# Kernel tuning notes

Measured on AMD Instinct MI355X. Metric: run time of the kernel, lower is better.

## Reference

```python
import jax, jax.numpy as jnp
import numpy as np

B, S, D, H = 4, 1024, 1024, 16
HS = D // H  # head_size = 64


def setup_inputs() -> dict:
    key = jax.random.key(0)
    ks = jax.random.split(key, 6)
    scale = 1.0 / np.sqrt(D)
    data = jax.random.normal(ks[0], (B, S, D), dtype=jnp.float32)
    # Per-head projection weights, stacked: [H, D, HS] (no bias, per nn.Linear(bias=False))
    Wq = jax.random.normal(ks[1], (H, D, HS), dtype=jnp.float32) * scale
    Wk = jax.random.normal(ks[2], (H, D, HS), dtype=jnp.float32) * scale
    Wv = jax.random.normal(ks[3], (H, D, HS), dtype=jnp.float32) * scale
    # Output projection: [H*HS, D] plus bias [D]
    Wo = jax.random.normal(ks[4], (H * HS, D), dtype=jnp.float32) * scale
    bo = jax.random.normal(ks[5], (D,), dtype=jnp.float32) * 0.01
    return {"data": data, "Wq": Wq, "Wk": Wk, "Wv": Wv, "Wo": Wo, "bo": bo}


def reference(data, Wq, Wk, Wv, Wo, bo):
    b, s, d = data.shape
    # Per-head Q/K/V projections (self-attention: encoder_data = data)
    q = jnp.einsum('bsd,hde->bhse', data, Wq)  # [B,H,S,HS]
    k = jnp.einsum('bsd,hde->bhse', data, Wk)
    v = jnp.einsum('bsd,hde->bhse', data, Wv)
    # NOTE: original scales by sqrt(embedding_dimension), not sqrt(head_size)
    scores = jnp.einsum('bhse,bhte->bhst', q, k) / jnp.sqrt(jnp.asarray(d, dtype=data.dtype))
    # causal mask (tril of block_size, sliced to [S, S])
    causal = jnp.tril(jnp.ones((s, s), dtype=bool))
    scores = jnp.where(causal, scores, -jnp.inf)
    attn = jax.nn.softmax(scores, axis=-1)  # dropout rate 0.0 -> identity
    out = jnp.einsum('bhst,bhte->bhse', attn, v)  # [B,H,S,HS]
    # concat heads along feature dim (head order matches ModuleList order)
    out = out.transpose(0, 2, 1, 3).reshape(b, s, -1)  # [B,S,H*HS]
    return out @ Wo + bo
```

## Files before the change

kernel.cpp:

```cpp
#include <hip/hip_runtime.h>
#include <hip/hip_bf16.h>
#include <stdint.h>

#define NEG_SENTINEL (-1e30f)

typedef short s16x8 __attribute__((ext_vector_type(8)));
typedef float f32x4 __attribute__((ext_vector_type(4)));

__device__ __forceinline__ ushort f2bf(float f) {
  union { float f; uint32_t u; } v; v.f = f;
  uint32_t u = v.u;
  u += 0x7fffu + ((u >> 16) & 1u);
  return (ushort)(u >> 16);
}
__device__ __forceinline__ ushort f2bf_rn(float f) {
  union { float f; uint32_t u; } v; v.f = f;
  return (ushort)((v.u + 0x8000u) >> 16);
}

__device__ __forceinline__ void async_ld16(ushort* lds, const ushort* g) {
  __builtin_amdgcn_global_load_lds(
      (const __attribute__((address_space(1))) uint32_t*)g,
      (__attribute__((address_space(3))) uint32_t*)lds, 16, 0, 0);
}

__global__ __launch_bounds__(256) void prep_kernel(
    const float* __restrict__ data, const float* __restrict__ Wq,
    const float* __restrict__ Wk, const float* __restrict__ Wv,
    const float* __restrict__ Wo, ushort* __restrict__ dataB,
    ushort* __restrict__ WTall, ushort* __restrict__ WoT) {
  const int blk = blockIdx.x;
  const int tid = threadIdx.x;
  if (blk < 2048) {
    long i = ((long)blk * 256 + tid) * 8;
    float4 a = *(const float4*)(data + i);
    float4 b = *(const float4*)(data + i + 4);
    union { ushort u[8]; uint4 v; } o;
    o.u[0] = f2bf(a.x); o.u[1] = f2bf(a.y); o.u[2] = f2bf(a.z); o.u[3] = f2bf(a.w);
    o.u[4] = f2bf(b.x); o.u[5] = f2bf(b.y); o.u[6] = f2bf(b.z); o.u[7] = f2bf(b.w);
    *(uint4*)(dataB + i) = o.v;
    return;
  }
  __shared__ __align__(16) ushort tile[64 * 72];
  const float* src;
  ushort* dst;
  int srcCols, dstRowStride, it, jt;
  if (blk < 2816) {
    int t = blk - 2048;
    int z = t >> 4;
    it = t & 15;  jt = 0;
    int matsel = z >> 4;
    src = (matsel == 0 ? Wq : (matsel == 1 ? Wk : Wv)) + (long)(z & 15) * 65536;
    dst = WTall + (long)z * 65536;
    srcCols = 64; dstRowStride = 1024;
  } else {
    int t = blk - 2816;
    jt = t & 15; it = t >> 4;
    src = Wo; dst = WoT;
    srcCols = 1024; dstRowStride = 1024;
  }
#pragma unroll
  for (int p = 0; p < 4; ++p) {
    int chunk = tid + p * 256;
    int r = chunk >> 4, c0 = (chunk & 15) * 4;
    float4 f = *(const float4*)(src + (long)(it * 64 + r) * srcCols + jt * 64 + c0);
    union { ushort u[4]; uint2 v; } o;
    o.u[0] = f2bf(f.x); o.u[1] = f2bf(f.y); o.u[2] = f2bf(f.z); o.u[3] = f2bf(f.w);
    *(uint2*)&tile[r * 72 + c0] = o.v;
  }
  __syncthreads();
#pragma unroll
  for (int p = 0; p < 2; ++p) {
    int chunk = tid + p * 256;
    int r = chunk >> 3, c0 = (chunk & 7) * 8;
    union { ushort u[8]; uint4 v; } tmp;
#pragma unroll
    for (int k2 = 0; k2 < 8; ++k2) tmp.u[k2] = tile[(c0 + k2) * 72 + r];
    *(uint4*)(dst + (long)(jt * 64 + r) * dstRowStride + it * 64 + c0) = tmp.v;
  }
}

__device__ __forceinline__ void gemm_core_128x128(
    const ushort* __restrict__ A, const ushort* __restrict__ BT,
    ushort* As, ushort* Bs, f32x4 acc[4][4]) {
  const int tid = threadIdx.x;
  const int lane = tid & 63, w = tid >> 6, quad = lane >> 4, l15 = lane & 15;
  const int wm = w >> 1, wn = w & 1;
  for (int k0 = 0; k0 < 1024; k0 += 64) {
#pragma unroll
    for (int p = 0; p < 4; ++p) {
      int c = tid + p * 256;
      int r = c >> 3, c8 = (c & 7) * 8;
      async_ld16(As + c * 8, A + (long)r * 1024 + k0 + c8);
      async_ld16(Bs + c * 8, BT + (long)r * 1024 + k0 + c8);
    }
    __syncthreads();
#pragma unroll
    for (int kk = 0; kk < 64; kk += 32) {
      s16x8 af[4], bfr[4];
#pragma unroll
      for (int mi = 0; mi < 4; ++mi)
        af[mi] = *(const s16x8*)&As[(wm * 64 + mi * 16 + l15) * 64 + kk + quad * 8];
#pragma unroll
      for (int ni = 0; ni < 4; ++ni)
        bfr[ni] = *(const s16x8*)&Bs[(wn * 64 + ni * 16 + l15) * 64 + kk + quad * 8];
#pragma unroll
      for (int mi = 0; mi < 4; ++mi)
#pragma unroll
        for (int ni = 0; ni < 4; ++ni)
          acc[mi][ni] = __builtin_amdgcn_mfma_f32_16x16x32_bf16(
              af[mi], bfr[ni], acc[mi][ni], 0, 0, 0);
    }
    __syncthreads();
  }
}

__global__ __launch_bounds__(256) void qkv_proj(
    const ushort* __restrict__ dataB, const ushort* __restrict__ WTall,
    ushort* __restrict__ QKV) {
  __shared__ __align__(16) ushort smem[128 * 136];
  ushort* As = smem;
  ushort* Bs = smem + 8192;
  ushort* Ct = smem;
  const int m0 = blockIdx.x * 128;
  const int n0 = blockIdx.y * 128;
  f32x4 acc[4][4];
  const f32x4 z = {0.f, 0.f, 0.f, 0.f};
#pragma unroll
  for (int mi = 0; mi < 4; ++mi)
#pragma unroll
    for (int ni = 0; ni < 4; ++ni) acc[mi][ni] = z;
  gemm_core_128x128(dataB + (long)m0 * 1024, WTall + (long)n0 * 1024, As, Bs, acc);

  const int tid = threadIdx.x;
  const int lane = tid & 63, w = tid >> 6, quad = lane >> 4, l15 = lane & 15;
  const int wm = w >> 1, wn = w & 1;
  const int matsel = n0 >> 10;
  const int bI = m0 >> 10, s0 = m0 & 1023;

  if (matsel < 2) {
    const float sc = (matsel == 0) ? 0.03125f : 1.0f;
    ushort* base = QKV + (long)matsel * 4194304 + (long)bI * 1048576;
#pragma unroll
    for (int mi = 0; mi < 4; ++mi) {
#pragma unroll
      for (int ni = 0; ni < 4; ++ni) {
        int n = n0 + wn * 64 + ni * 16 + l15;
        int h = (n >> 6) & 15, e = n & 63;
        ushort* col = base + (long)h * 65536 + e;
#pragma unroll
        for (int i = 0; i < 4; ++i) {
          int s = s0 + wm * 64 + mi * 16 + quad * 4 + i;
          col[s * 64] = f2bf(acc[mi][ni][i] * sc);
        }
      }
    }
  } else {
#pragma unroll
    for (int mi = 0; mi < 4; ++mi)
#pragma unroll
      for (int ni = 0; ni < 4; ++ni)
#pragma unroll
        for (int i = 0; i < 4; ++i)
          Ct[(wn * 64 + ni * 16 + l15) * 136 + wm * 64 + mi * 16 + quad * 4 + i] =
              f2bf(acc[mi][ni][i]);
    __syncthreads();
    ushort* base = QKV + 8388608 + (long)bI * 1048576;
#pragma unroll
    for (int p = 0; p < 8; ++p) {
      int c = tid + p * 256;
      int r = c >> 4, m8 = (c & 15) * 8;
      int h = ((n0 + r) >> 6) & 15, e = (n0 + r) & 63;
      *(uint4*)(base + (long)h * 65536 + e * 1024 + s0 + m8) =
          *(const uint4*)&Ct[r * 136 + m8];
    }
  }
}

__global__ __launch_bounds__(256) void out_proj(
    const ushort* __restrict__ Ocat, const ushort* __restrict__ WoT,
    const float* __restrict__ bo, float* __restrict__ out) {
  __shared__ __align__(16) ushort As[128 * 64];
  __shared__ __align__(16) ushort Bs[128 * 64];
  const int m0 = blockIdx.x * 128;
  const int n0 = blockIdx.y * 128;
  f32x4 acc[4][4];
  const f32x4 z = {0.f, 0.f, 0.f, 0.f};
#pragma unroll
  for (int mi = 0; mi < 4; ++mi)
#pragma unroll
    for (int ni = 0; ni < 4; ++ni) acc[mi][ni] = z;
  gemm_core_128x128(Ocat + (long)m0 * 1024, WoT + (long)n0 * 1024, As, Bs, acc);

  const int tid = threadIdx.x;
  const int lane = tid & 63, w = tid >> 6, quad = lane >> 4, l15 = lane & 15;
  const int wm = w >> 1, wn = w & 1;
#pragma unroll
  for (int mi = 0; mi < 4; ++mi) {
#pragma unroll
    for (int ni = 0; ni < 4; ++ni) {
#pragma unroll
      for (int i = 0; i < 4; ++i) {
        int m = m0 + wm * 64 + mi * 16 + quad * 4 + i;
        int n = n0 + wn * 64 + ni * 16 + l15;
        out[(long)m * 1024 + n] = acc[mi][ni][i] + bo[n];
      }
    }
  }
}

__global__ __launch_bounds__(256, 2) void attn_kernel(
    const ushort* __restrict__ QKV, ushort* __restrict__ Ocat) {
  __shared__ __align__(16) ushort Ks[128 * 72];
  __shared__ __align__(16) ushort Vs[64 * 136];
  __shared__ __align__(16) ushort Ps[4 * 16 * 136];
  const int bh = blockIdx.x;
  const int b = bh >> 4, h = bh & 15;
  const int tid = threadIdx.x;
  const int w = tid >> 6, lane = tid & 63, quad = lane >> 4, l15 = lane & 15;

  const ushort* Qp = QKV + (long)bh * 65536;
  const ushort* Kp = QKV + 4194304 + (long)bh * 65536;
  const ushort* VTp = QKV + 8388608 + (long)bh * 65536;
  ushort* Psw = Ps + w * (16 * 136);
  const f32x4 z = {0.f, 0.f, 0.f, 0.f};

#pragma unroll
  for (int phase = 0; phase < 2; ++phase) {
    const int qt = phase == 0 ? (int)blockIdx.y : 15 - (int)blockIdx.y;
    const int q0 = qt * 64;
    const int nj = (qt >> 1) + 1;

    const int qrow = q0 + w * 16 + l15;
    s16x8 qf0 = *(const s16x8*)(Qp + (long)qrow * 64 + quad * 8);
    s16x8 qf1 = *(const s16x8*)(Qp + (long)qrow * 64 + 32 + quad * 8);

    f32x4 oacc[4];
#pragma unroll
    for (int et = 0; et < 4; ++et) oacc[et] = z;
    float l_i[4] = {0.f, 0.f, 0.f, 0.f};

    for (int j = 0; j < nj; ++j) {
#pragma unroll
      for (int p = 0; p < 4; ++p) {
        int c = tid + p * 256;
        { int r = c >> 3, c8 = (c & 7) * 8;
          *(uint4*)&Ks[r * 72 + c8] =
              *(const uint4*)(Kp + (long)(j * 128 + r) * 64 + c8); }
        { int r = c >> 4, c8 = (c & 15) * 8;
          *(uint4*)&Vs[r * 136 + c8] =
              *(const uint4*)(VTp + (long)r * 1024 + j * 128 + c8); }
      }
      __syncthreads();

      f32x4 sacc[8];
#pragma unroll
      for (int nt = 0; nt < 8; ++nt) sacc[nt] = z;
#pragma unroll
      for (int kk = 0; kk < 64; kk += 32) {
        s16x8 a = kk ? qf1 : qf0;
#pragma unroll
        for (int nt = 0; nt < 8; ++nt) {
          s16x8 bfr = *(const s16x8*)&Ks[(nt * 16 + l15) * 72 + kk + quad * 8];
          sacc[nt] = __builtin_amdgcn_mfma_f32_16x16x32_bf16(a, bfr, sacc[nt], 0, 0, 0);
        }
      }

      if (j == nj - 1) {
        const int srow = q0 + w * 16 + quad * 4;
#pragma unroll
        for (int nt = 0; nt < 8; ++nt) {
#pragma unroll
          for (int i = 0; i < 4; ++i) {
            int tg = j * 128 + nt * 16 + l15;
            if (tg > srow + i) sacc[nt][i] = NEG_SENTINEL;
          }
        }
      }

#pragma unroll
      for (int i = 0; i < 4; ++i) {
#pragma unroll
        for (int nt = 0; nt < 8; ++nt) {
          float p = __expf(sacc[nt][i]);
          Psw[(quad * 4 + i) * 136 + nt * 16 + l15] = f2bf_rn(p);
          l_i[i] += p;
        }
      }

#pragma unroll
      for (int kk = 0; kk < 128; kk += 32) {
        s16x8 pa = *(const s16x8*)&Psw[l15 * 136 + kk + quad * 8];
#pragma unroll
        for (int et = 0; et < 4; ++et) {
          s16x8 vb = *(const s16x8*)&Vs[(et * 16 + l15) * 136 + kk + quad * 8];
          oacc[et] = __builtin_amdgcn_mfma_f32_16x16x32_bf16(pa, vb, oacc[et], 0, 0, 0);
        }
      }
      __syncthreads();
    }

#pragma unroll
    for (int i = 0; i < 4; ++i) {
#pragma unroll
      for (int d = 1; d < 16; d <<= 1) l_i[i] += __shfl_xor(l_i[i], d, 64);
    }
    ushort* Ob = Ocat + ((long)(b * 1024 + q0 + w * 16) * 1024) + h * 64;
#pragma unroll
    for (int et = 0; et < 4; ++et) {
#pragma unroll
      for (int i = 0; i < 4; ++i) {
        float denom = l_i[i];
        float v = oacc[et][i] / (denom > 0.f ? denom : 1.0f);
        Ob[(long)(quad * 4 + i) * 1024 + et * 16 + l15] = f2bf_rn(v);
      }
    }
  }
}

extern "C" void kernel_launch(void* const* d_in, const int* in_sizes, int n_in,
                              void* d_out, int out_size, void* d_ws, size_t ws_size,
                              hipStream_t stream) {
  const float* data = (const float*)d_in[0];
  const float* Wq = (const float*)d_in[1];
  const float* Wk = (const float*)d_in[2];
  const float* Wv = (const float*)d_in[3];
  const float* Wo = (const float*)d_in[4];
  const float* bo = (const float*)d_in[5];
  float* out = (float*)d_out;

  ushort* ws = (ushort*)d_ws;
  ushort* QKV = ws;
  ushort* dataB = ws + 12582912;
  ushort* Ocat = ws + 16777216;
  ushort* WTall = ws + 20971520;
  ushort* WoT = ws + 20971520 + 3145728;

  dim3 blk(256);
  prep_kernel<<<dim3(3072), blk, 0, stream>>>(data, Wq, Wk, Wv, Wo,
                                              dataB, WTall, WoT);
  qkv_proj<<<dim3(32, 24), blk, 0, stream>>>(dataB, WTall, QKV);
  attn_kernel<<<dim3(64, 8), blk, 0, stream>>>(QKV, Ocat);
  out_proj<<<dim3(32, 8), blk, 0, stream>>>(Ocat, WoT, bo, out);
}
```

Before: 186.9 us.

## Fuse all four stages into one persistent kernel with grid barriers

Replaces the four separate launches (prep, QKV projection, attention, output projection) with one persistent 512-block kernel. Stages are separated by atomic-counter grid barriers, and the GEMM stages pull tiles from atomic work queues. This removes per-launch overhead and the gaps between kernels, but adds a memset, spin-wait barriers that depend on all 512 blocks being resident at once, and forces every stage to run at the same occupancy and shared-memory footprint. Ocat now aliases the dataB buffer.

```diff
diff --git a/kernel.cpp b/kernel.cpp
--- a/kernel.cpp
+++ b/kernel.cpp
@@ -24,13 +24,27 @@
       (__attribute__((address_space(3))) uint32_t*)lds, 16, 0, 0);
 }
 
-__global__ __launch_bounds__(256) void prep_kernel(
-    const float* __restrict__ data, const float* __restrict__ Wq,
-    const float* __restrict__ Wk, const float* __restrict__ Wv,
-    const float* __restrict__ Wo, ushort* __restrict__ dataB,
-    ushort* __restrict__ WTall, ushort* __restrict__ WoT) {
-  const int blk = blockIdx.x;
-  const int tid = threadIdx.x;
+__device__ void grid_barrier(uint32_t* cnt, uint32_t target) {
+  __syncthreads();
+  if (threadIdx.x == 0) {
+    __threadfence();
+    __hip_atomic_fetch_add(cnt, 1u, __ATOMIC_ACQ_REL, __HIP_MEMORY_SCOPE_AGENT);
+    uint32_t guard = 0;
+    while (__hip_atomic_load(cnt, __ATOMIC_ACQUIRE,
+                             __HIP_MEMORY_SCOPE_AGENT) < target) {
+      __builtin_amdgcn_s_sleep(32);
+      if (++guard > (1u << 21)) break;
+    }
+    __threadfence();
+  }
+  __syncthreads();
+}
+
+__device__ void prep_unit(int blk, int tid, const float* __restrict__ data,
+                          const float* __restrict__ Wq, const float* __restrict__ Wk,
+                          const float* __restrict__ Wv, const float* __restrict__ Wo,
+                          ushort* __restrict__ dataB, ushort* __restrict__ WTall,
+                          ushort* __restrict__ WoT, ushort* tile) {
   if (blk < 2048) {
     long i = ((long)blk * 256 + tid) * 8;
     float4 a = *(const float4*)(data + i);
@@ -41,7 +55,6 @@
     *(uint4*)(dataB + i) = o.v;
     return;
   }
-  __shared__ __align__(16) ushort tile[64 * 72];
   const float* src;
   ushort* dst;
   int srcCols, dstRowStride, it, jt;
@@ -115,15 +128,14 @@
   }
 }
 
-__global__ __launch_bounds__(256) void qkv_proj(
-    const ushort* __restrict__ dataB, const ushort* __restrict__ WTall,
-    ushort* __restrict__ QKV) {
-  __shared__ __align__(16) ushort smem[128 * 136];
+__device__ void qkv_tile(int t, const ushort* __restrict__ dataB,
+                         const ushort* __restrict__ WTall,
+                         ushort* __restrict__ QKV, ushort* smem) {
   ushort* As = smem;
   ushort* Bs = smem + 8192;
   ushort* Ct = smem;
-  const int m0 = blockIdx.x * 128;
-  const int n0 = blockIdx.y * 128;
+  const int m0 = (t & 31) * 128;
+  const int n0 = (t >> 5) * 128;
   f32x4 acc[4][4];
   const f32x4 z = {0.f, 0.f, 0.f, 0.f};
 #pragma unroll
@@ -177,13 +189,14 @@
   }
 }
 
-__global__ __launch_bounds__(256) void out_proj(
-    const ushort* __restrict__ Ocat, const ushort* __restrict__ WoT,
-    const float* __restrict__ bo, float* __restrict__ out) {
-  __shared__ __align__(16) ushort As[128 * 64];
-  __shared__ __align__(16) ushort Bs[128 * 64];
-  const int m0 = blockIdx.x * 128;
-  const int n0 = blockIdx.y * 128;
+__device__ void out_tile(int t, const ushort* __restrict__ Ocat,
+                         const ushort* __restrict__ WoT,
+                         const float* __restrict__ bo, float* __restrict__ out,
+                         ushort* smem) {
+  ushort* As = smem;
+  ushort* Bs = smem + 8192;
+  const int m0 = (t & 31) * 128;
+  const int n0 = (t >> 5) * 128;
   f32x4 acc[4][4];
   const f32x4 z = {0.f, 0.f, 0.f, 0.f};
 #pragma unroll
@@ -209,12 +222,11 @@
   }
 }
 
-__global__ __launch_bounds__(256, 2) void attn_kernel(
-    const ushort* __restrict__ QKV, ushort* __restrict__ Ocat) {
-  __shared__ __align__(16) ushort Ks[128 * 72];
-  __shared__ __align__(16) ushort Vs[64 * 136];
-  __shared__ __align__(16) ushort Ps[4 * 16 * 136];
-  const int bh = blockIdx.x;
+__device__ void attn_block(int bh, int y, const ushort* __restrict__ QKV,
+                           ushort* __restrict__ Ocat, ushort* smem) {
+  ushort* Ks = smem;
+  ushort* Vs = smem + 9216;
+  ushort* Ps = smem + 17920;
   const int b = bh >> 4, h = bh & 15;
   const int tid = threadIdx.x;
   const int w = tid >> 6, lane = tid & 63, quad = lane >> 4, l15 = lane & 15;
@@ -227,7 +239,7 @@
 
 #pragma unroll
   for (int phase = 0; phase < 2; ++phase) {
-    const int qt = phase == 0 ? (int)blockIdx.y : 15 - (int)blockIdx.y;
+    const int qt = phase == 0 ? y : 15 - y;
     const int q0 = qt * 64;
     const int nj = (qt >> 1) + 1;
 
@@ -315,6 +327,57 @@
         Ob[(long)(quad * 4 + i) * 1024 + et * 16 + l15] = f2bf_rn(v);
       }
     }
+  }
+}
+
+__global__ __launch_bounds__(256, 2) void mega_kernel(
+    const float* __restrict__ data, const float* __restrict__ Wq,
+    const float* __restrict__ Wk, const float* __restrict__ Wv,
+    const float* __restrict__ Wo, const float* __restrict__ bo,
+    float* __restrict__ out, ushort* __restrict__ ws) {
+  __shared__ __align__(16) ushort smem[26624];
+  __shared__ int curT;
+  const int bid = blockIdx.x;
+  const int tid = threadIdx.x;
+
+  ushort* QKV = ws;
+  ushort* dataB = ws + 12582912;
+  ushort* Ocat = ws + 12582912;
+  uint32_t* sync = (uint32_t*)(ws + 16777216);
+  ushort* WTall = ws + 20971520;
+  ushort* WoT = ws + 20971520 + 3145728;
+
+#pragma unroll
+  for (int i = 0; i < 6; ++i) {
+    prep_unit(bid + 512 * i, tid, data, Wq, Wk, Wv, Wo, dataB, WTall, WoT, smem);
+    __syncthreads();
+  }
+  grid_barrier(&sync[0], 512);
+
+  for (;;) {
+    if (tid == 0)
+      curT = (int)__hip_atomic_fetch_add(&sync[24], 1u, __ATOMIC_RELAXED,
+                                         __HIP_MEMORY_SCOPE_AGENT);
+    __syncthreads();
+    int t = curT;
+    if (t >= 768) break;
+    qkv_tile(t, dataB, WTall, QKV, smem);
+    __syncthreads();
+  }
+  grid_barrier(&sync[8], 512);
+
+  attn_block(bid >> 3, bid & 7, QKV, Ocat, smem);
+  grid_barrier(&sync[16], 512);
+
+  for (;;) {
+    if (tid == 0)
+      curT = (int)__hip_atomic_fetch_add(&sync[28], 1u, __ATOMIC_RELAXED,
+                                         __HIP_MEMORY_SCOPE_AGENT);
+    __syncthreads();
+    int t = curT;
+    if (t >= 256) break;
+    out_tile(t, Ocat, WoT, bo, out, smem);
+    __syncthreads();
   }
 }
 
@@ -328,18 +391,9 @@
   const float* Wo = (const float*)d_in[4];
   const float* bo = (const float*)d_in[5];
   float* out = (float*)d_out;
-
-  ushort* ws = (ushort*)d_ws;
-  ushort* QKV = ws;
-  ushort* dataB = ws + 12582912;
-  ushort* Ocat = ws + 16777216;
-  ushort* WTall = ws + 20971520;
-  ushort* WoT = ws + 20971520 + 3145728;
-
-  dim3 blk(256);
-  prep_kernel<<<dim3(3072), blk, 0, stream>>>(data, Wq, Wk, Wv, Wo,
-                                              dataB, WTall, WoT);
-  qkv_proj<<<dim3(32, 24), blk, 0, stream>>>(dataB, WTall, QKV);
-  attn_kernel<<<dim3(64, 8), blk, 0, stream>>>(QKV, Ocat);
-  out_proj<<<dim3(32, 8), blk, 0, stream>>>(Ocat, WoT, bo, out);
-}
+  ushort* wsp = (ushort*)d_ws;
+
+  hipMemsetAsync((char*)d_ws + 33554432, 0, 128, stream);
+  mega_kernel<<<dim3(512), dim3(256), 0, stream>>>(data, Wq, Wk, Wv, Wo, bo,
+                                                   out, wsp);
+}
```

New measurement: 525.5 us. 2.81x slower.
